# Optimization experiments

Measured on AMD Instinct MI355X. Metric: run time of the kernel, lower is better.

The kernel has to match this reference:

```python
import jax, jax.numpy as jnp
import numpy as np

ALPHA, BETA, GAMMA = 1.0, 0.01, 0.1
COS_EPS = 1e-8  # torch F.cosine_similarity eps


def setup_inputs() -> dict:
    key = jax.random.key(0)
    k1, k2, k3, k4 = jax.random.split(key, 4)
    B, C = 4096, 1000
    N, D = 8192, 256
    return {
        "pred": jax.random.normal(k1, (B, C), dtype=jnp.float32),
        "target": jax.random.randint(k2, (B,), 0, C, dtype=jnp.int64),
        "adj_matrix": jax.random.uniform(k3, (N, N), dtype=jnp.float32),
        "node_embeddings": jax.random.normal(k4, (N, D), dtype=jnp.float32),
    }


def reference(pred, target, adj_matrix, node_embeddings):
    # L_task: mean cross-entropy over logits
    logp = jax.nn.log_softmax(pred, axis=-1)                      # [B, C]
    l_task = -jnp.mean(jnp.take_along_axis(logp, target[:, None], axis=1))

    # L_sparse: mean |adj|
    l_sparse = jnp.mean(jnp.abs(adj_matrix))

    # L_semantic: cosine similarity via normalize + matmul (avoids NxNxD intermediate)
    norms = jnp.linalg.norm(node_embeddings, axis=1)              # [N]
    dots = node_embeddings @ node_embeddings.T                    # [N, N]
    sim = dots / jnp.maximum(norms[:, None] * norms[None, :], COS_EPS)
    l_semantic = jnp.mean(adj_matrix * (1.0 - sim))

    return ALPHA * l_task + BETA * l_sparse + GAMMA * l_semantic
```

## Files before the change

kernel.cpp:

```cpp
#include <hip/hip_runtime.h>
#include <hip/hip_bf16.h>
#include <stdint.h>
#include <stddef.h>

#define N_NODES 8192
#define DIM     256
#define BATCH   4096
#define CLASSES 1000
#define ALPHA_C 1.0f
#define BETA_C  0.01f
#define GAMMA_C 0.1f

#define KSPLIT  16
#define KRANGE  (N_NODES / KSPLIT)
#define SUPER   256
#define NSUPER  (KRANGE / SUPER)
#define BK      64
#define NBK     (SUPER / BK)
#define BM      64

typedef __bf16 bf16_t;
typedef __bf16 bf16x4 __attribute__((ext_vector_type(4)));
typedef __bf16 bf16x8 __attribute__((ext_vector_type(8)));
typedef float  f32x4  __attribute__((ext_vector_type(4)));
typedef float  f32x16 __attribute__((ext_vector_type(16)));

__device__ __forceinline__ void async16(const void* g, void* l) {
  __builtin_amdgcn_global_load_lds(
      (const __attribute__((address_space(1))) uint32_t*)g,
      (__attribute__((address_space(3))) uint32_t*)l, 16, 0, 0);
}

__global__ __launch_bounds__(256) void prep_norm(
    const float* __restrict__ emb, bf16_t* __restrict__ U) {
  const int row = blockIdx.x;
  const int t = threadIdx.x;
  const float v = emb[(size_t)row * DIM + t];
  float sq = v * v;
  for (int off = 32; off; off >>= 1) sq += __shfl_down(sq, off);
  __shared__ float red[4];
  if ((t & 63) == 0) red[t >> 6] = sq;
  __syncthreads();
  const float total = red[0] + red[1] + red[2] + red[3];
  U[(size_t)row * DIM + t] = (bf16_t)(v * rsqrtf(total));
}

#define TP 68

__global__ __launch_bounds__(256) void prep_transpose(
    const bf16_t* __restrict__ U, bf16_t* __restrict__ V) {
  __shared__ bf16_t tile[64 * TP];
  const int k0 = blockIdx.x * 64;
  const int d0 = blockIdx.y * 64;
  const int t = threadIdx.x;
  const int r = t >> 3;
  const int c8 = t & 7;

  *(bf16x8*)&tile[r * TP + c8 * 8] =
      *(const bf16x8*)&U[(size_t)(k0 + r) * DIM + d0 + c8 * 8];
  *(bf16x8*)&tile[(r + 32) * TP + c8 * 8] =
      *(const bf16x8*)&U[(size_t)(k0 + r + 32) * DIM + d0 + c8 * 8];
  __syncthreads();

  bf16x8 o0, o1;
#pragma unroll
  for (int j = 0; j < 8; ++j) {
    o0[j] = tile[(c8 * 8 + j) * TP + r];
    o1[j] = tile[(c8 * 8 + j) * TP + r + 32];
  }
  *(bf16x8*)&V[(size_t)(d0 + r) * N_NODES + k0 + c8 * 8] = o0;
  *(bf16x8*)&V[(size_t)(d0 + r + 32) * N_NODES + k0 + c8 * 8] = o1;
}

__global__ __launch_bounds__(256) void ce_kernel(
    const float* __restrict__ pred, const int* __restrict__ target,
    float* __restrict__ out) {
  const int row = blockIdx.x;
  const int t = threadIdx.x;
  const float* p = pred + (size_t)row * CLASSES;

  float v[4];
  for (int k = 0; k < 4; ++k) {
    const int c = t + k * 256;
    v[k] = (c < CLASSES) ? p[c] : -INFINITY;
  }

  float m = fmaxf(fmaxf(v[0], v[1]), fmaxf(v[2], v[3]));
  for (int off = 32; off; off >>= 1) m = fmaxf(m, __shfl_down(m, off));

  __shared__ float red[8];
  const int wave = t >> 6, lane = t & 63;
  if (lane == 0) red[wave] = m;
  __syncthreads();
  if (t == 0) red[4] = fmaxf(fmaxf(red[0], red[1]), fmaxf(red[2], red[3]));
  __syncthreads();
  const float mx = red[4];

  float s = 0.f;
  for (int k = 0; k < 4; ++k) s += __expf(v[k] - mx);
  for (int off = 32; off; off >>= 1) s += __shfl_down(s, off);
  if (lane == 0) red[wave] = s;
  __syncthreads();
  if (t == 0) {
    float ssum = red[0] + red[1] + red[2] + red[3];
    float lse = mx + __logf(ssum);
    float loss = lse - p[target[row]];
    atomicAdd(out, loss * (ALPHA_C / (float)BATCH));
  }
}

__global__ __launch_bounds__(256, 2) void gemm_kernel(
    const float* __restrict__ adj, const bf16_t* __restrict__ U,
    const bf16_t* __restrict__ V, float* __restrict__ out) {
  __shared__ __align__(16) bf16_t As[BM * SUPER];
  __shared__ __align__(16) bf16_t Bs[DIM * BK];
  __shared__ float red[4];

  const int i0 = blockIdx.x * BM;
  const int kbase = blockIdx.y * KRANGE;
  const int t = threadIdx.x;
  const int w = t >> 6, lane = t & 63;
  const int m = lane & 31, h = lane >> 5;
  const int srow = lane >> 3;
  const int sch = (lane & 7) ^ srow;

  const float* arow =
      adj + (size_t)(i0 + w * 16) * N_NODES + kbase + lane * 4;
  float4 pf0[16], pf1[16];
#pragma unroll
  for (int j = 0; j < 16; ++j)
    pf0[j] = *(const float4*)(arow + (size_t)j * N_NODES);
#pragma unroll
  for (int j = 0; j < 16; ++j)
    pf1[j] = *(const float4*)(arow + (size_t)j * N_NODES + SUPER);

  f32x16 acc[2][2] = {};
  float sa = 0.f, sabs = 0.f;

#pragma unroll
  for (int s = 0; s < NSUPER; ++s) {
    __syncthreads();

#pragma unroll
    for (int j = 0; j < 16; ++j) {
      const float4 v = s ? pf1[j] : pf0[j];
      sa += v.x + v.y + v.z + v.w;
      sabs += fabsf(v.x) + fabsf(v.y) + fabsf(v.z) + fabsf(v.w);
      const int r = w * 16 + j;
      bf16x4 c;
      c[0] = (bf16_t)v.x; c[1] = (bf16_t)v.y;
      c[2] = (bf16_t)v.z; c[3] = (bf16_t)v.w;
      const int pos = (((lane >> 1) ^ (r & 31)) & 31) * 8 + (lane & 1) * 4;
      *(bf16x4*)&As[r * SUPER + pos] = c;
    }

#pragma unroll
    for (int bk = 0; bk < NBK; ++bk) {
      const int k0 = kbase + s * SUPER + bk * BK;
#pragma unroll
      for (int q = 0; q < 8; ++q) {
        const int dbase = w * 64 + q * 8;
        async16(V + (size_t)(dbase + srow) * N_NODES + k0 + sch * 8,
                &Bs[dbase * 64]);
      }
      __syncthreads();

#pragma unroll
      for (int kk = 0; kk < 4; ++kk) {
        const int qa = bk * 8 + kk * 2 + h;
        const int pa = ((qa ^ m) & 31) * 8;
        bf16x8 a0 = *(const bf16x8*)&As[m * SUPER + pa];
        bf16x8 a1 = *(const bf16x8*)&As[(m + 32) * SUPER + pa];
        const int pb = ((kk * 2 + h) ^ (m & 7)) * 8;
        bf16x8 b0 = *(const bf16x8*)&Bs[(w * 64 + m) * 64 + pb];
        bf16x8 b1 = *(const bf16x8*)&Bs[(w * 64 + 32 + m) * 64 + pb];
        acc[0][0] = __builtin_amdgcn_mfma_f32_32x32x16_bf16(a0, b0, acc[0][0],
                                                            0, 0, 0);
        acc[0][1] = __builtin_amdgcn_mfma_f32_32x32x16_bf16(a0, b1, acc[0][1],
                                                            0, 0, 0);
        acc[1][0] = __builtin_amdgcn_mfma_f32_32x32x16_bf16(a1, b0, acc[1][0],
                                                            0, 0, 0);
        acc[1][1] = __builtin_amdgcn_mfma_f32_32x32x16_bf16(a1, b1, acc[1][1],
                                                            0, 0, 0);
      }
    }
  }

  float simdot = 0.f;
#pragma unroll
  for (int mi = 0; mi < 2; ++mi) {
#pragma unroll
    for (int nd = 0; nd < 2; ++nd) {
      const int ib = i0 + mi * 32 + 4 * h;
      const int d = w * 64 + nd * 32 + m;
      const bf16_t* up = U + (size_t)ib * DIM + d;
#pragma unroll
      for (int rg = 0; rg < 16; ++rg) {
        const int row = (rg & 3) + 8 * (rg >> 2);
        simdot += (float)up[(size_t)row * DIM] * acc[mi][nd][rg];
      }
    }
  }

  float local = BETA_C * sabs + GAMMA_C * (sa - simdot);
  for (int off = 32; off; off >>= 1) local += __shfl_down(local, off);
  if (lane == 0) red[w] = local;
  __syncthreads();
  if (t == 0) {
    const float inv = 1.f / ((float)N_NODES * (float)N_NODES);
    atomicAdd(out, (red[0] + red[1] + red[2] + red[3]) * inv);
  }
}

extern "C" void kernel_launch(void* const* d_in, const int* in_sizes, int n_in,
                              void* d_out, int out_size, void* d_ws,
                              size_t ws_size, hipStream_t stream) {
  const float* pred   = (const float*)d_in[0];
  const int*   target = (const int*)d_in[1];
  const float* adj    = (const float*)d_in[2];
  const float* emb    = (const float*)d_in[3];
  float* out = (float*)d_out;

  bf16_t* U = (bf16_t*)d_ws;
  bf16_t* V = (bf16_t*)((char*)d_ws + (size_t)N_NODES * DIM * 2);

  hipMemsetAsync(d_out, 0, sizeof(float), stream);
  ce_kernel<<<BATCH, 256, 0, stream>>>(pred, target, out);
  prep_norm<<<N_NODES, 256, 0, stream>>>(emb, U);
  prep_transpose<<<dim3(N_NODES / 64, DIM / 64), 256, 0, stream>>>(U, V);
  gemm_kernel<<<dim3(N_NODES / BM, KSPLIT), 256, 0, stream>>>(adj, U, V, out);
}
```

Measured before the change: 506.8 us.

## Double-buffer V tiles and shrink row tile with fewer k-splits in fused GEMM

New measurement: 504.8 us. About the same (-0.4%).

```diff
diff --git a/kernel.cpp b/kernel.cpp
--- a/kernel.cpp
+++ b/kernel.cpp
@@ -11,18 +11,15 @@
 #define BETA_C  0.01f
 #define GAMMA_C 0.1f
 
-#define KSPLIT  16
+#define BM      32
+#define KSPLIT  2
 #define KRANGE  (N_NODES / KSPLIT)
 #define SUPER   256
-#define NSUPER  (KRANGE / SUPER)
-#define BK      64
-#define NBK     (SUPER / BK)
-#define BM      64
+#define NSUP    (KRANGE / SUPER)
 
 typedef __bf16 bf16_t;
 typedef __bf16 bf16x4 __attribute__((ext_vector_type(4)));
 typedef __bf16 bf16x8 __attribute__((ext_vector_type(8)));
-typedef float  f32x4  __attribute__((ext_vector_type(4)));
 typedef float  f32x16 __attribute__((ext_vector_type(16)));
 
 __device__ __forceinline__ void async16(const void* g, void* l) {
@@ -109,96 +106,109 @@
   }
 }
 
-__global__ __launch_bounds__(256, 2) void gemm_kernel(
+__global__ __launch_bounds__(256) void gemm_kernel(
     const float* __restrict__ adj, const bf16_t* __restrict__ U,
     const bf16_t* __restrict__ V, float* __restrict__ out) {
   __shared__ __align__(16) bf16_t As[BM * SUPER];
-  __shared__ __align__(16) bf16_t Bs[DIM * BK];
+  __shared__ __align__(16) bf16_t Bs[2][DIM * 64];
   __shared__ float red[4];
 
-  const int i0 = blockIdx.x * BM;
-  const int kbase = blockIdx.y * KRANGE;
+  const int bx = blockIdx.x, by = blockIdx.y;
+  const int i0 = bx * BM;
+  const int kbase = by * KRANGE;
   const int t = threadIdx.x;
   const int w = t >> 6, lane = t & 63;
   const int m = lane & 31, h = lane >> 5;
   const int srow = lane >> 3;
-  const int sch = (lane & 7) ^ srow;
-
-  const float* arow =
-      adj + (size_t)(i0 + w * 16) * N_NODES + kbase + lane * 4;
-  float4 pf0[16], pf1[16];
-#pragma unroll
-  for (int j = 0; j < 16; ++j)
-    pf0[j] = *(const float4*)(arow + (size_t)j * N_NODES);
-#pragma unroll
-  for (int j = 0; j < 16; ++j)
-    pf1[j] = *(const float4*)(arow + (size_t)j * N_NODES + SUPER);
-
-  f32x16 acc[2][2] = {};
+  const int sch = (lane & 7) ^ (srow & 7);
+  const int sstart = (bx * 5 + by * 7) & (NSUP - 1);
+
+  const float* arow = adj + (size_t)(i0 + w * 8) * N_NODES + lane * 4;
+
+  auto issueB = [&](int buf, int k0) {
+#pragma unroll
+    for (int q = 0; q < 8; ++q) {
+      const int dbase = w * 64 + q * 8;
+      async16(V + (size_t)(dbase + srow) * N_NODES + k0 + sch * 8,
+              &Bs[buf][dbase * 64]);
+    }
+  };
+
+  f32x16 acc[2] = {};
+
+  auto compute = [&](int buf, int bk) {
+#pragma unroll
+    for (int kk = 0; kk < 4; ++kk) {
+      const int qa = bk * 8 + kk * 2 + h;
+      const int pa = ((qa ^ m) & 31) * 8;
+      bf16x8 a0 = *(const bf16x8*)&As[m * SUPER + pa];
+      const int pb = ((kk * 2 + h) ^ (m & 7)) * 8;
+      bf16x8 b0 = *(const bf16x8*)&Bs[buf][(w * 64 + m) * 64 + pb];
+      bf16x8 b1 = *(const bf16x8*)&Bs[buf][(w * 64 + 32 + m) * 64 + pb];
+      acc[0] = __builtin_amdgcn_mfma_f32_32x32x16_bf16(a0, b0, acc[0], 0, 0, 0);
+      acc[1] = __builtin_amdgcn_mfma_f32_32x32x16_bf16(a0, b1, acc[1], 0, 0, 0);
+    }
+  };
+
   float sa = 0.f, sabs = 0.f;
 
-#pragma unroll
-  for (int s = 0; s < NSUPER; ++s) {
+  float4 pf[8];
+  {
+    const int ks = kbase + sstart * SUPER;
+#pragma unroll
+    for (int j = 0; j < 8; ++j)
+      pf[j] = *(const float4*)(arow + (size_t)j * N_NODES + ks);
+  }
+
+  for (int si = 0; si < NSUP; ++si) {
+    const int s = (sstart + si) & (NSUP - 1);
+    const int ks = kbase + s * SUPER;
+
     __syncthreads();
 
-#pragma unroll
-    for (int j = 0; j < 16; ++j) {
-      const float4 v = s ? pf1[j] : pf0[j];
+    issueB(0, ks);
+
+#pragma unroll
+    for (int j = 0; j < 8; ++j) {
+      const float4 v = pf[j];
       sa += v.x + v.y + v.z + v.w;
       sabs += fabsf(v.x) + fabsf(v.y) + fabsf(v.z) + fabsf(v.w);
-      const int r = w * 16 + j;
+      const int r = w * 8 + j;
       bf16x4 c;
       c[0] = (bf16_t)v.x; c[1] = (bf16_t)v.y;
       c[2] = (bf16_t)v.z; c[3] = (bf16_t)v.w;
       const int pos = (((lane >> 1) ^ (r & 31)) & 31) * 8 + (lane & 1) * 4;
       *(bf16x4*)&As[r * SUPER + pos] = c;
     }
-
-#pragma unroll
-    for (int bk = 0; bk < NBK; ++bk) {
-      const int k0 = kbase + s * SUPER + bk * BK;
-#pragma unroll
-      for (int q = 0; q < 8; ++q) {
-        const int dbase = w * 64 + q * 8;
-        async16(V + (size_t)(dbase + srow) * N_NODES + k0 + sch * 8,
-                &Bs[dbase * 64]);
-      }
-      __syncthreads();
-
-#pragma unroll
-      for (int kk = 0; kk < 4; ++kk) {
-        const int qa = bk * 8 + kk * 2 + h;
-        const int pa = ((qa ^ m) & 31) * 8;
-        bf16x8 a0 = *(const bf16x8*)&As[m * SUPER + pa];
-        bf16x8 a1 = *(const bf16x8*)&As[(m + 32) * SUPER + pa];
-        const int pb = ((kk * 2 + h) ^ (m & 7)) * 8;
-        bf16x8 b0 = *(const bf16x8*)&Bs[(w * 64 + m) * 64 + pb];
-        bf16x8 b1 = *(const bf16x8*)&Bs[(w * 64 + 32 + m) * 64 + pb];
-        acc[0][0] = __builtin_amdgcn_mfma_f32_32x32x16_bf16(a0, b0, acc[0][0],
-                                                            0, 0, 0);
-        acc[0][1] = __builtin_amdgcn_mfma_f32_32x32x16_bf16(a0, b1, acc[0][1],
-                                                            0, 0, 0);
-        acc[1][0] = __builtin_amdgcn_mfma_f32_32x32x16_bf16(a1, b0, acc[1][0],
-                                                            0, 0, 0);
-        acc[1][1] = __builtin_amdgcn_mfma_f32_32x32x16_bf16(a1, b1, acc[1][1],
-                                                            0, 0, 0);
-      }
-    }
+    __syncthreads();
+
+    issueB(1, ks + 64);
+    compute(0, 0);
+    __builtin_amdgcn_s_waitcnt(0x0f70);
+    issueB(0, ks + 128);
+    compute(1, 1);
+    __builtin_amdgcn_s_waitcnt(0x0f70);
+    issueB(1, ks + 192);
+    compute(0, 2);
+    __builtin_amdgcn_s_waitcnt(0x0f70);
+    if (si + 1 < NSUP) {
+      const int kn = kbase + ((sstart + si + 1) & (NSUP - 1)) * SUPER;
+#pragma unroll
+      for (int j = 0; j < 8; ++j)
+        pf[j] = *(const float4*)(arow + (size_t)j * N_NODES + kn);
+    }
+    compute(1, 3);
   }
 
   float simdot = 0.f;
 #pragma unroll
-  for (int mi = 0; mi < 2; ++mi) {
-#pragma unroll
-    for (int nd = 0; nd < 2; ++nd) {
-      const int ib = i0 + mi * 32 + 4 * h;
-      const int d = w * 64 + nd * 32 + m;
-      const bf16_t* up = U + (size_t)ib * DIM + d;
-#pragma unroll
-      for (int rg = 0; rg < 16; ++rg) {
-        const int row = (rg & 3) + 8 * (rg >> 2);
-        simdot += (float)up[(size_t)row * DIM] * acc[mi][nd][rg];
-      }
+  for (int nd = 0; nd < 2; ++nd) {
+    const int d = w * 64 + nd * 32 + m;
+    const bf16_t* up = U + (size_t)(i0 + 4 * h) * DIM + d;
+#pragma unroll
+    for (int rg = 0; rg < 16; ++rg) {
+      const int row = (rg & 3) + 8 * (rg >> 2);
+      simdot += (float)up[(size_t)row * DIM] * acc[nd][rg];
     }
   }
 
```

## Split adjacency conversion into a streaming bf16 pass before the GEMM

Applied to the files above, without the earlier changes.

Result: slower. 531.3 us (+4.9%).

```diff
diff --git a/kernel.cpp b/kernel.cpp
--- a/kernel.cpp
+++ b/kernel.cpp
@@ -13,16 +13,11 @@
 
 #define KSPLIT  16
 #define KRANGE  (N_NODES / KSPLIT)
-#define SUPER   256
-#define NSUPER  (KRANGE / SUPER)
-#define BK      64
-#define NBK     (SUPER / BK)
+#define NBK     (KRANGE / 64)
 #define BM      64
 
 typedef __bf16 bf16_t;
-typedef __bf16 bf16x4 __attribute__((ext_vector_type(4)));
 typedef __bf16 bf16x8 __attribute__((ext_vector_type(8)));
-typedef float  f32x4  __attribute__((ext_vector_type(4)));
 typedef float  f32x16 __attribute__((ext_vector_type(16)));
 
 __device__ __forceinline__ void async16(const void* g, void* l) {
@@ -109,11 +104,46 @@
   }
 }
 
-__global__ __launch_bounds__(256, 2) void gemm_kernel(
-    const float* __restrict__ adj, const bf16_t* __restrict__ U,
+#define SBLK 4096
+
+__global__ __launch_bounds__(256, 8) void stream_cvt(
+    const float* __restrict__ adj, bf16_t* __restrict__ Abf,
+    float* __restrict__ out) {
+  const int gi = blockIdx.x * 256 + threadIdx.x;
+  float sa = 0.f, sabs = 0.f;
+
+#pragma unroll
+  for (int it = 0; it < 8; ++it) {
+    const size_t P = (size_t)it * (SBLK * 256) + gi;
+    const float4 v0 = *(const float4*)(adj + P * 8);
+    const float4 v1 = *(const float4*)(adj + P * 8 + 4);
+    sa += v0.x + v0.y + v0.z + v0.w + v1.x + v1.y + v1.z + v1.w;
+    sabs += fabsf(v0.x) + fabsf(v0.y) + fabsf(v0.z) + fabsf(v0.w) +
+            fabsf(v1.x) + fabsf(v1.y) + fabsf(v1.z) + fabsf(v1.w);
+    bf16x8 c;
+    c[0] = (bf16_t)v0.x; c[1] = (bf16_t)v0.y;
+    c[2] = (bf16_t)v0.z; c[3] = (bf16_t)v0.w;
+    c[4] = (bf16_t)v1.x; c[5] = (bf16_t)v1.y;
+    c[6] = (bf16_t)v1.z; c[7] = (bf16_t)v1.w;
+    *(bf16x8*)(Abf + P * 8) = c;
+  }
+
+  float local = BETA_C * sabs + GAMMA_C * sa;
+  for (int off = 32; off; off >>= 1) local += __shfl_down(local, off);
+  __shared__ float red[4];
+  if ((threadIdx.x & 63) == 0) red[threadIdx.x >> 6] = local;
+  __syncthreads();
+  if (threadIdx.x == 0) {
+    const float inv = 1.f / ((float)N_NODES * (float)N_NODES);
+    atomicAdd(out, (red[0] + red[1] + red[2] + red[3]) * inv);
+  }
+}
+
+__global__ __launch_bounds__(256, 4) void gemm_kernel(
+    const bf16_t* __restrict__ Abf, const bf16_t* __restrict__ U,
     const bf16_t* __restrict__ V, float* __restrict__ out) {
-  __shared__ __align__(16) bf16_t As[BM * SUPER];
-  __shared__ __align__(16) bf16_t Bs[DIM * BK];
+  __shared__ __align__(16) bf16_t As[BM * 64];
+  __shared__ __align__(16) bf16_t Bs[DIM * 64];
   __shared__ float red[4];
 
   const int i0 = blockIdx.x * BM;
@@ -124,66 +154,42 @@
   const int srow = lane >> 3;
   const int sch = (lane & 7) ^ srow;
 
-  const float* arow =
-      adj + (size_t)(i0 + w * 16) * N_NODES + kbase + lane * 4;
-  float4 pf0[16], pf1[16];
-#pragma unroll
-  for (int j = 0; j < 16; ++j)
-    pf0[j] = *(const float4*)(arow + (size_t)j * N_NODES);
-#pragma unroll
-  for (int j = 0; j < 16; ++j)
-    pf1[j] = *(const float4*)(arow + (size_t)j * N_NODES + SUPER);
-
   f32x16 acc[2][2] = {};
-  float sa = 0.f, sabs = 0.f;
-
-#pragma unroll
-  for (int s = 0; s < NSUPER; ++s) {
+
+  for (int bk = 0; bk < NBK; ++bk) {
+    const int k0 = kbase + bk * 64;
+
+#pragma unroll
+    for (int q = 0; q < 2; ++q) {
+      const int rbase = w * 16 + q * 8;
+      async16(Abf + (size_t)(i0 + rbase + srow) * N_NODES + k0 + sch * 8,
+              &As[rbase * 64]);
+    }
+#pragma unroll
+    for (int q = 0; q < 8; ++q) {
+      const int dbase = w * 64 + q * 8;
+      async16(V + (size_t)(dbase + srow) * N_NODES + k0 + sch * 8,
+              &Bs[dbase * 64]);
+    }
     __syncthreads();
 
 #pragma unroll
-    for (int j = 0; j < 16; ++j) {
-      const float4 v = s ? pf1[j] : pf0[j];
-      sa += v.x + v.y + v.z + v.w;
-      sabs += fabsf(v.x) + fabsf(v.y) + fabsf(v.z) + fabsf(v.w);
-      const int r = w * 16 + j;
-      bf16x4 c;
-      c[0] = (bf16_t)v.x; c[1] = (bf16_t)v.y;
-      c[2] = (bf16_t)v.z; c[3] = (bf16_t)v.w;
-      const int pos = (((lane >> 1) ^ (r & 31)) & 31) * 8 + (lane & 1) * 4;
-      *(bf16x4*)&As[r * SUPER + pos] = c;
-    }
-
-#pragma unroll
-    for (int bk = 0; bk < NBK; ++bk) {
-      const int k0 = kbase + s * SUPER + bk * BK;
-#pragma unroll
-      for (int q = 0; q < 8; ++q) {
-        const int dbase = w * 64 + q * 8;
-        async16(V + (size_t)(dbase + srow) * N_NODES + k0 + sch * 8,
-                &Bs[dbase * 64]);
-      }
-      __syncthreads();
-
-#pragma unroll
-      for (int kk = 0; kk < 4; ++kk) {
-        const int qa = bk * 8 + kk * 2 + h;
-        const int pa = ((qa ^ m) & 31) * 8;
-        bf16x8 a0 = *(const bf16x8*)&As[m * SUPER + pa];
-        bf16x8 a1 = *(const bf16x8*)&As[(m + 32) * SUPER + pa];
-        const int pb = ((kk * 2 + h) ^ (m & 7)) * 8;
-        bf16x8 b0 = *(const bf16x8*)&Bs[(w * 64 + m) * 64 + pb];
-        bf16x8 b1 = *(const bf16x8*)&Bs[(w * 64 + 32 + m) * 64 + pb];
-        acc[0][0] = __builtin_amdgcn_mfma_f32_32x32x16_bf16(a0, b0, acc[0][0],
-                                                            0, 0, 0);
-        acc[0][1] = __builtin_amdgcn_mfma_f32_32x32x16_bf16(a0, b1, acc[0][1],
-                                                            0, 0, 0);
-        acc[1][0] = __builtin_amdgcn_mfma_f32_32x32x16_bf16(a1, b0, acc[1][0],
-                                                            0, 0, 0);
-        acc[1][1] = __builtin_amdgcn_mfma_f32_32x32x16_bf16(a1, b1, acc[1][1],
-                                                            0, 0, 0);
-      }
-    }
+    for (int kk = 0; kk < 4; ++kk) {
+      const int p = ((kk * 2 + h) ^ (m & 7)) * 8;
+      bf16x8 a0 = *(const bf16x8*)&As[m * 64 + p];
+      bf16x8 a1 = *(const bf16x8*)&As[(m + 32) * 64 + p];
+      bf16x8 b0 = *(const bf16x8*)&Bs[(w * 64 + m) * 64 + p];
+      bf16x8 b1 = *(const bf16x8*)&Bs[(w * 64 + 32 + m) * 64 + p];
+      acc[0][0] = __builtin_amdgcn_mfma_f32_32x32x16_bf16(a0, b0, acc[0][0],
+                                                          0, 0, 0);
+      acc[0][1] = __builtin_amdgcn_mfma_f32_32x32x16_bf16(a0, b1, acc[0][1],
+                                                          0, 0, 0);
+      acc[1][0] = __builtin_amdgcn_mfma_f32_32x32x16_bf16(a1, b0, acc[1][0],
+                                                          0, 0, 0);
+      acc[1][1] = __builtin_amdgcn_mfma_f32_32x32x16_bf16(a1, b1, acc[1][1],
+                                                          0, 0, 0);
+    }
+    __syncthreads();
   }
 
   float simdot = 0.f;
@@ -202,7 +208,7 @@
     }
   }
 
-  float local = BETA_C * sabs + GAMMA_C * (sa - simdot);
+  float local = -GAMMA_C * simdot;
   for (int off = 32; off; off >>= 1) local += __shfl_down(local, off);
   if (lane == 0) red[w] = local;
   __syncthreads();
@@ -221,12 +227,14 @@
   const float* emb    = (const float*)d_in[3];
   float* out = (float*)d_out;
 
-  bf16_t* U = (bf16_t*)d_ws;
-  bf16_t* V = (bf16_t*)((char*)d_ws + (size_t)N_NODES * DIM * 2);
+  bf16_t* U   = (bf16_t*)d_ws;
+  bf16_t* V   = (bf16_t*)((char*)d_ws + (size_t)4 * 1024 * 1024);
+  bf16_t* Abf = (bf16_t*)((char*)d_ws + (size_t)8 * 1024 * 1024);
 
   hipMemsetAsync(d_out, 0, sizeof(float), stream);
   ce_kernel<<<BATCH, 256, 0, stream>>>(pred, target, out);
   prep_norm<<<N_NODES, 256, 0, stream>>>(emb, U);
   prep_transpose<<<dim3(N_NODES / 64, DIM / 64), 256, 0, stream>>>(U, V);
-  gemm_kernel<<<dim3(N_NODES / BM, KSPLIT), 256, 0, stream>>>(adj, U, V, out);
-}
+  stream_cvt<<<SBLK, 256, 0, stream>>>(adj, Abf, out);
+  gemm_kernel<<<dim3(N_NODES / BM, KSPLIT), 256, 0, stream>>>(Abf, U, V, out);
+}
```
